# Kernel optimization log

Hardware: AMD Instinct MI355X
Metric: run time of the kernel (lower is better)

## Reference

```python
import jax, jax.numpy as jnp
import numpy as np

B, T, C, HS = 1024, 128, 384, 64


def setup_inputs() -> dict:
    key = jax.random.key(0)
    k1, k2, k3, k4 = jax.random.split(key, 4)
    std = 1.0 / np.sqrt(C)  # ~ nn.Linear default init scale
    return {
        "x": jax.random.normal(k1, (B, T, C), dtype=jnp.float32),
        "Wq": jax.random.normal(k2, (C, HS), dtype=jnp.float32) * std,
        "Wk": jax.random.normal(k3, (C, HS), dtype=jnp.float32) * std,
        "Wv": jax.random.normal(k4, (C, HS), dtype=jnp.float32) * std,
    }


def reference(x, Wq, Wk, Wv):
    # x: [B, T, C]; Wq/Wk/Wv: [C, HS]
    q = jnp.einsum("btc,ch->bth", x, Wq)
    k = jnp.einsum("btc,ch->bth", x, Wk)
    v = jnp.einsum("btc,ch->bth", x, Wv)
    scale = 1.0 / jnp.sqrt(jnp.asarray(k.shape[-1], dtype=x.dtype))
    wei = jnp.einsum("bth,bsh->bts", q, k) * scale  # [B, T, T]
    t = x.shape[1]
    causal = jnp.tril(jnp.ones((t, t), dtype=bool))
    wei = jnp.where(causal, wei, jnp.asarray(-jnp.inf, dtype=wei.dtype))
    wei = jax.nn.softmax(wei, axis=-1)
    # dropout omitted (eval mode / deterministic reference)
    out = jnp.einsum("bts,bsh->bth", wei, v)  # [B, T, HS]
    return out
```

## Files before the change

### kernel.cpp

```cpp
#include <hip/hip_runtime.h>


typedef __attribute__((ext_vector_type(8)))  short  short8;
typedef __attribute__((ext_vector_type(16))) float  floatx16;
typedef __attribute__((ext_vector_type(4)))  float  float4v;

#define T_DIM   128
#define C_DIM   384
#define HS      64
#define NCHUNK  12
#define SLAB    1536

#define QK_PITCH 68
#define V_PITCH  132
#define P_PITCH  132
#define Q_OFF 0
#define K_OFF 17408
#define V_OFF 34816
#define LDS_BYTES 51712
#define P_OFF 0

#define MFMA(a,b,c) __builtin_amdgcn_mfma_f32_32x32x16_bf16((a),(b),(c),0,0,0)

__device__ inline unsigned short f2bf(float f){
    unsigned u = __builtin_bit_cast(unsigned, f);
    u += 0x7FFFu + ((u >> 16) & 1u);
    return (unsigned short)(u >> 16);
}

__device__ inline short8 ld_b64x2(const char* p){
    union { unsigned long long u[2]; short8 s; } r;
    r.u[0] = *(const unsigned long long*)(p);
    r.u[1] = *(const unsigned long long*)(p + 8);
    return r.s;
}

__global__ void prep_wt(const float* __restrict__ Wq, const float* __restrict__ Wk,
                        const float* __restrict__ Wv, unsigned short* __restrict__ wt){
    int idx = blockIdx.x * 256 + threadIdx.x;
    if (idx >= 48 * SLAB) return;
    int slab = idx / SLAB;
    int rem  = idx - slab * SLAB;
    int n = rem >> 3, j = rem & 7;
    int half = slab & 1, ks = (slab >> 1) & 1, c = slab >> 2;
    int kg = c*32 + ks*16 + half*8 + j;
    const float* W = (n < 64) ? Wq : (n < 128) ? Wk : Wv;
    wt[idx] = f2bf(W[kg * HS + (n & 63)]);
}

__launch_bounds__(256, 3)
__global__ void attn_kernel(const float* __restrict__ x,
                            const unsigned short* __restrict__ wtg,
                            float* __restrict__ out){
    __shared__ __align__(16) char smem[LDS_BYTES];
    const int tid  = threadIdx.x;
    const int lane = tid & 63;
    const int wave = tid >> 6;
    const int l31  = lane & 31;
    const int half = lane >> 5;
    const int koff = half * 8;
    const int b    = blockIdx.x;
    const float* xb = x + (size_t)b * (T_DIM * C_DIM);

    const float* xrow = xb + (32*wave + l31) * C_DIM;
    const short8* wf = (const short8*)wtg;

    floatx16 acc[6] = {};
    float4v bufA[4], bufB[4];

    auto xload = [&](float4v (&buf)[4], int c){
        #pragma unroll
        for (int ks = 0; ks < 2; ++ks){
            const float* g = xrow + (c*32 + ks*16 + koff);
            buf[ks*2+0] = *(const float4v*)g;
            buf[ks*2+1] = *(const float4v*)(g + 4);
        }
    };
    auto body = [&](int c, float4v (&cur)[4], float4v (&nxt)[4]){
        if (c + 1 < NCHUNK) xload(nxt, c + 1);
        short8 afrag[2];
        #pragma unroll
        for (int ks = 0; ks < 2; ++ks){
            float4v lo = cur[ks*2+0], hi = cur[ks*2+1];
            short8 a;
            a[0]=(short)f2bf(lo[0]); a[1]=(short)f2bf(lo[1]);
            a[2]=(short)f2bf(lo[2]); a[3]=(short)f2bf(lo[3]);
            a[4]=(short)f2bf(hi[0]); a[5]=(short)f2bf(hi[1]);
            a[6]=(short)f2bf(hi[2]); a[7]=(short)f2bf(hi[3]);
            afrag[ks] = a;
        }
        #pragma unroll
        for (int ks = 0; ks < 2; ++ks){
            const short8* slab = wf + ((c*2 + ks)*2 + half) * 192;
            #pragma unroll
            for (int nbl = 0; nbl < 6; ++nbl){
                short8 bfrag = slab[32*nbl + l31];
                acc[nbl] = MFMA(afrag[ks], bfrag, acc[nbl]);
            }
        }
    };

    xload(bufA, 0);
    for (int cc = 0; cc < NCHUNK; cc += 2){
        body(cc,     bufA, bufB);
        body(cc + 1, bufB, bufA);
    }

    const float QSCALE = 0.125f * 1.44269504088896f;
    #pragma unroll
    for (int nb = 0; nb < 6; ++nb){
        floatx16 A = acc[nb];
        if (nb < 4){
            int base  = (nb < 2) ? Q_OFF : K_OFF;
            int col   = 32 * (nb & 1) + l31;
            float sc  = (nb < 2) ? QSCALE : 1.0f;
            char* bp  = smem + base + col * 2;
            #pragma unroll
            for (int r = 0; r < 16; ++r){
                int t = 32*wave + (r&3) + 8*(r>>2) + 4*half;
                *(unsigned short*)(bp + t * (QK_PITCH*2)) = f2bf(A[r] * sc);
            }
        } else {
            int h = 32*(nb-4) + l31;
            char* bp = smem + V_OFF + h * (V_PITCH*2);
            #pragma unroll
            for (int g = 0; g < 4; ++g){
                int t0 = 32*wave + 8*g + 4*half;
                union { unsigned short s[4]; unsigned long long u; } pk;
                pk.s[0]=f2bf(A[4*g+0]); pk.s[1]=f2bf(A[4*g+1]);
                pk.s[2]=f2bf(A[4*g+2]); pk.s[3]=f2bf(A[4*g+3]);
                *(unsigned long long*)(bp + t0*2) = pk.u;
            }
        }
    }
    __syncthreads();

    floatx16 accS[4] = {};
    #pragma unroll
    for (int ks = 0; ks < 4; ++ks){
        short8 aq = ld_b64x2(smem + Q_OFF + (32*wave + l31)*(QK_PITCH*2) + (ks*16 + koff)*2);
        #pragma unroll
        for (int st = 0; st < 4; ++st)
            if (st <= wave){
                short8 bk = ld_b64x2(smem + K_OFF + (32*st + l31)*(QK_PITCH*2) + (ks*16 + koff)*2);
                accS[st] = MFMA(aq, bk, accS[st]);
            }
    }
    #pragma unroll
    for (int st = 0; st < 4; ++st)
        if (st <= wave){
            #pragma unroll
            for (int r = 0; r < 16; ++r){
                int trow = (r&3) + 8*(r>>2) + 4*half;
                float e = exp2f(accS[st][r]);
                if (st == wave && l31 > trow) e = 0.0f;
                accS[st][r] = e;
            }
        }

    float linv[16];
    #pragma unroll
    for (int r = 0; r < 16; ++r){
        float l = accS[0][r] + accS[1][r] + accS[2][r] + accS[3][r];
        #pragma unroll
        for (int m = 1; m <= 16; m <<= 1)
            l += __shfl_xor(l, m);
        linv[r] = 1.0f / l;
    }
    __syncthreads();

    #pragma unroll
    for (int st = 0; st < 4; ++st)
        if (st <= wave){
            char* bp = smem + P_OFF + (32*st + l31) * 2;
            #pragma unroll
            for (int r = 0; r < 16; ++r){
                int t = 32*wave + (r&3) + 8*(r>>2) + 4*half;
                *(unsigned short*)(bp + t * (P_PITCH*2)) = f2bf(accS[st][r]);
            }
        }
    __syncthreads();

    floatx16 accO0 = {}, accO1 = {};
    const int nks = 2 * (wave + 1);
    #pragma unroll
    for (int ks = 0; ks < 8; ++ks)
        if (ks < nks){
            short8 ap  = ld_b64x2(smem + P_OFF + (32*wave + l31)*(P_PITCH*2) + (ks*16 + koff)*2);
            short8 bv0 = ld_b64x2(smem + V_OFF + l31        *(V_PITCH*2) + (ks*16 + koff)*2);
            short8 bv1 = ld_b64x2(smem + V_OFF + (l31 + 32) *(V_PITCH*2) + (ks*16 + koff)*2);
            accO0 = MFMA(ap, bv0, accO0);
            accO1 = MFMA(ap, bv1, accO1);
        }

    float* ob = out + (size_t)b * (T_DIM * HS);
    #pragma unroll
    for (int r = 0; r < 16; ++r){
        int t = 32*wave + (r&3) + 8*(r>>2) + 4*half;
        ob[t*HS + l31]      = accO0[r] * linv[r];
        ob[t*HS + l31 + 32] = accO1[r] * linv[r];
    }
}

extern "C" void kernel_launch(void* const* d_in, const int* in_sizes, int n_in,
                              void* d_out, int out_size, void* d_ws, size_t ws_size,
                              hipStream_t stream){
    const float* x  = (const float*)d_in[0];
    const float* Wq = (const float*)d_in[1];
    const float* Wk = (const float*)d_in[2];
    const float* Wv = (const float*)d_in[3];
    unsigned short* wt = (unsigned short*)d_ws;

    prep_wt<<<288, 256, 0, stream>>>(Wq, Wk, Wv, wt);
    attn_kernel<<<1024, 256, 0, stream>>>(x, wt, (float*)d_out);
}
```

Measured before the change: 329.1 us.

## Stage x chunks through LDS via global_load_lds with XOR swizzle

Replaces per-thread register double-buffered global loads of x with direct global-to-LDS async loads (global_load_lds) into a swizzled region shared with V. Each wave then reads its fp32 row fragments from LDS before converting to bf16 for MFMA. The aim is coalesced, fully-line loads of x and lower VGPR pressure. In exchange it drops the register prefetch overlap, adding two block barriers per chunk, which serializes loading and compute.

```diff
diff --git a/kernel.cpp b/kernel.cpp
--- a/kernel.cpp
+++ b/kernel.cpp
@@ -14,11 +14,11 @@
 #define QK_PITCH 68
 #define V_PITCH  132
 #define P_PITCH  132
-#define Q_OFF 0
-#define K_OFF 17408
-#define V_OFF 34816
+#define Q_OFF  0
+#define K_OFF  17408
+#define XV_OFF 34816
 #define LDS_BYTES 51712
-#define P_OFF 0
+#define P_OFF  0
 
 #define MFMA(a,b,c) __builtin_amdgcn_mfma_f32_32x32x16_bf16((a),(b),(c),0,0,0)
 
@@ -60,28 +60,39 @@
     const int half = lane >> 5;
     const int koff = half * 8;
     const int b    = blockIdx.x;
-    const float* xb = x + (size_t)b * (T_DIM * C_DIM);
-
-    const float* xrow = xb + (32*wave + l31) * C_DIM;
+    const char* xb = (const char*)(x + (size_t)b * (T_DIM * C_DIM));
+
     const short8* wf = (const short8*)wtg;
-
     floatx16 acc[6] = {};
-    float4v bufA[4], bufB[4];
-
-    auto xload = [&](float4v (&buf)[4], int c){
+
+    const char* gsrc[4];
+    #pragma unroll
+    for (int i = 0; i < 4; ++i){
+        int o  = wave*1024 + i*4096 + lane*16;
+        int t  = o >> 7;
+        int pp = ((o >> 4) & 7) ^ (t & 7);
+        gsrc[i] = xb + t*1536 + pp*16;
+    }
+    const int xrow_base = XV_OFF + (32*wave + l31) * 128;
+    const int rs = (32*wave + l31) & 7;
+
+    for (int c = 0; c < NCHUNK; ++c){
+        __syncthreads();
+        #pragma unroll
+        for (int i = 0; i < 4; ++i){
+            __builtin_amdgcn_global_load_lds(
+                (const __attribute__((address_space(1))) void*)(gsrc[i] + c*128),
+                (__attribute__((address_space(3))) void*)(smem + XV_OFF + wave*1024 + i*4096),
+                16, 0, 0);
+        }
+        __syncthreads();
+
+        short8 afrag[2];
         #pragma unroll
         for (int ks = 0; ks < 2; ++ks){
-            const float* g = xrow + (c*32 + ks*16 + koff);
-            buf[ks*2+0] = *(const float4v*)g;
-            buf[ks*2+1] = *(const float4v*)(g + 4);
-        }
-    };
-    auto body = [&](int c, float4v (&cur)[4], float4v (&nxt)[4]){
-        if (c + 1 < NCHUNK) xload(nxt, c + 1);
-        short8 afrag[2];
-        #pragma unroll
-        for (int ks = 0; ks < 2; ++ks){
-            float4v lo = cur[ks*2+0], hi = cur[ks*2+1];
+            int q0 = ks*4 + half*2;
+            float4v lo = *(const float4v*)(smem + xrow_base + ((q0  ) ^ rs)*16);
+            float4v hi = *(const float4v*)(smem + xrow_base + ((q0+1) ^ rs)*16);
             short8 a;
             a[0]=(short)f2bf(lo[0]); a[1]=(short)f2bf(lo[1]);
             a[2]=(short)f2bf(lo[2]); a[3]=(short)f2bf(lo[3]);
@@ -98,13 +109,8 @@
                 acc[nbl] = MFMA(afrag[ks], bfrag, acc[nbl]);
             }
         }
-    };
-
-    xload(bufA, 0);
-    for (int cc = 0; cc < NCHUNK; cc += 2){
-        body(cc,     bufA, bufB);
-        body(cc + 1, bufB, bufA);
-    }
+    }
+    __syncthreads();
 
     const float QSCALE = 0.125f * 1.44269504088896f;
     #pragma unroll
@@ -122,7 +128,7 @@
             }
         } else {
             int h = 32*(nb-4) + l31;
-            char* bp = smem + V_OFF + h * (V_PITCH*2);
+            char* bp = smem + XV_OFF + h * (V_PITCH*2);
             #pragma unroll
             for (int g = 0; g < 4; ++g){
                 int t0 = 32*wave + 8*g + 4*half;
@@ -187,8 +193,8 @@
     for (int ks = 0; ks < 8; ++ks)
         if (ks < nks){
             short8 ap  = ld_b64x2(smem + P_OFF + (32*wave + l31)*(P_PITCH*2) + (ks*16 + koff)*2);
-            short8 bv0 = ld_b64x2(smem + V_OFF + l31        *(V_PITCH*2) + (ks*16 + koff)*2);
-            short8 bv1 = ld_b64x2(smem + V_OFF + (l31 + 32) *(V_PITCH*2) + (ks*16 + koff)*2);
+            short8 bv0 = ld_b64x2(smem + XV_OFF + l31        *(V_PITCH*2) + (ks*16 + koff)*2);
+            short8 bv1 = ld_b64x2(smem + XV_OFF + (l31 + 32) *(V_PITCH*2) + (ks*16 + koff)*2);
             accO0 = MFMA(ap, bv0, accO0);
             accO1 = MFMA(ap, bv1, accO1);
         }
```

Result: faster. 317.3 us (-3.6%).
